# Performance work log

Measured on AMD Instinct MI355X. Metric: run time of the kernel, lower is better.

Reference implementation:

```python
import jax, jax.numpy as jnp
import numpy as np

B, T, E = 4, 2048, 1024
HS = 64            # attention_head_size
NH = E // HS       # num_heads = 16 (all heads share one weight set in the original)


def setup_inputs() -> dict:
    key = jax.random.key(0)
    ks = jax.random.split(key, 6)
    s = 0.02
    x = jax.random.normal(ks[0], (B, T, E), dtype=jnp.float32)
    Wq = jax.random.normal(ks[1], (E, HS), dtype=jnp.float32) * s
    Wk = jax.random.normal(ks[2], (E, HS), dtype=jnp.float32) * s
    Wv = jax.random.normal(ks[3], (E, HS), dtype=jnp.float32) * s
    Wp = jax.random.normal(ks[4], (E, E), dtype=jnp.float32) * s
    bp = jax.random.normal(ks[5], (E,), dtype=jnp.float32) * s
    return {"x": x, "Wq": Wq, "Wk": Wk, "Wv": Wv, "Wp": Wp, "bp": bp}


def reference(x, Wq, Wk, Wv, Wp, bp):
    # Single shared head (the torch module replicates one Head instance NH times).
    hs = Wq.shape[1]
    num_heads = Wp.shape[0] // hs
    q = jnp.einsum('bte,eh->bth', x, Wq)   # [B,T,HS]
    k = jnp.einsum('bte,eh->bth', x, Wk)
    v = jnp.einsum('bte,eh->bth', x, Wv)
    att = jnp.einsum('bqh,bkh->bqk', q, k) * (hs ** -0.5)  # [B,T,T]
    t = x.shape[1]
    causal = jnp.tril(jnp.ones((t, t), dtype=bool))
    att = jnp.where(causal, att, jnp.finfo(att.dtype).min)
    att = jax.nn.softmax(att, axis=-1)
    head = jnp.einsum('bqk,bkh->bqh', att, v)              # [B,T,HS]
    # Concat of identical head outputs == tile along feature dim.
    out = jnp.tile(head, (1, 1, num_heads))                # [B,T,E]
    out = jnp.einsum('bte,ef->btf', out, Wp) + bp          # output projection
    return out
```

## Files before the change

### kernel.cpp

```cpp
#include <hip/hip_runtime.h>
#include <hip/hip_bf16.h>

#define T_SEQ 2048
#define E_DIM 1024
#define HSZ   64
#define NBAT  4
#define QB    64
#define NQT   32

typedef __attribute__((ext_vector_type(8))) short short8;
typedef __attribute__((ext_vector_type(4))) float f32x4;

__device__ inline short f2bf(float f) {
  union { float f; unsigned u; } v; v.f = f;
  unsigned r = v.u + 0x7FFFu + ((v.u >> 16) & 1u);
  return (short)(r >> 16);
}

__global__ __launch_bounds__(256) void wpr_kernel(const float* __restrict__ Wp,
                                                  short* __restrict__ Wpb) {
  int idx = blockIdx.x * 256 + threadIdx.x;
  int f = idx & (E_DIM - 1);
  int j = idx >> 10;
  float s = 0.f;
#pragma unroll
  for (int h = 0; h < 16; ++h) s += Wp[(size_t)(h * HSZ + j) * E_DIM + f];
  Wpb[(size_t)f * HSZ + j] = f2bf(s);
}

__global__ __launch_bounds__(256) void wt_kernel(const float* __restrict__ Wq,
    const float* __restrict__ Wk, const float* __restrict__ Wv,
    short* __restrict__ Wt) {
  int idx = blockIdx.x * 256 + threadIdx.x;
  int kk = idx & 63;
  int tmp = idx >> 6;
  int kt = tmp / 192;
  int n = tmp - kt * 192;
  const float* W = (n < 64) ? Wq : (n < 128) ? Wk : Wv;
  Wt[idx] = f2bf(W[(size_t)(kt * 64 + kk) * HSZ + (n & 63)]);
}

__global__ __launch_bounds__(256) void qkv_mfma(const float* __restrict__ X,
    const short* __restrict__ Wt, short* __restrict__ Qo,
    short* __restrict__ Ko, short* __restrict__ Vt) {
  __shared__ short Xs[16 * 64];
  __shared__ short Ws[192 * 64];

  const int tid = threadIdx.x;
  const int m0 = blockIdx.x * 16;
  const int lane = tid & 63, w = tid >> 6;
  const int l15 = lane & 15, l4 = lane >> 4;

  f32x4 acc[3];
  acc[0] = (f32x4)0.f; acc[1] = (f32x4)0.f; acc[2] = (f32x4)0.f;

  for (int kt = 0; kt < 16; ++kt) {
    const int k0 = kt * 64;
    if (tid < 128) {
      int r = tid >> 3, c = tid & 7;
      const float* s = &X[(size_t)(m0 + r) * E_DIM + k0 + c * 8];
      float4 a = *(const float4*)s, d = *(const float4*)(s + 4);
      short8 f;
      f[0] = f2bf(a.x); f[1] = f2bf(a.y); f[2] = f2bf(a.z); f[3] = f2bf(a.w);
      f[4] = f2bf(d.x); f[5] = f2bf(d.y); f[6] = f2bf(d.z); f[7] = f2bf(d.w);
      *(short8*)&Xs[r * 64 + ((c ^ (r & 7)) * 8)] = f;
    }
    {
      const short* wsrc = Wt + (size_t)kt * 12288;
#pragma unroll
      for (int i = 0; i < 6; ++i) {
        int ci = tid + i * 256;
        int r = ci >> 3, c = ci & 7;
        short8 f = *(const short8*)&wsrc[ci * 8];
        *(short8*)&Ws[r * 64 + ((c ^ (r & 7)) * 8)] = f;
      }
    }
    __syncthreads();
#pragma unroll
    for (int ks = 0; ks < 2; ++ks) {
      short8 af = *(short8*)&Xs[l15 * 64 + (((ks * 4 + l4) ^ (l15 & 7)) * 8)];
#pragma unroll
      for (int i = 0; i < 3; ++i) {
        int n = (w * 3 + i) * 16 + l15;
        short8 bf = *(short8*)&Ws[n * 64 + (((ks * 4 + l4) ^ (n & 7)) * 8)];
        acc[i] = __builtin_amdgcn_mfma_f32_16x16x32_bf16(af, bf, acc[i], 0, 0, 0);
      }
    }
    __syncthreads();
  }

  const int b = m0 >> 11, t = m0 & 2047;
#pragma unroll
  for (int i = 0; i < 3; ++i) {
    const int nb = w * 3 + i;
    const int col = (nb & 3) * 16 + l15;
    const int sel = nb >> 2;
#pragma unroll
    for (int reg = 0; reg < 4; ++reg) {
      const int row = l4 * 4 + reg;
      short v = f2bf(acc[i][reg]);
      if (sel == 0)      Qo[(size_t)(m0 + row) * HSZ + col] = v;
      else if (sel == 1) Ko[(size_t)(m0 + row) * HSZ + col] = v;
      else               Vt[((size_t)b * HSZ + col) * T_SEQ + t + row] = v;
    }
  }
}

__global__ __launch_bounds__(256) void attn_part(const short* __restrict__ Q,
    const short* __restrict__ K, const short* __restrict__ Vt,
    float* __restrict__ Opart, float* __restrict__ mpart,
    float* __restrict__ lpart, int splits) {
  const int qt = blockIdx.x;
  const int sp = blockIdx.y;
  const int b  = blockIdx.z;
  const int ntile = qt + 1;
  const int t0 = (sp * ntile) / splits;
  const int t1 = ((sp + 1) * ntile) / splits;
  const int q0 = qt * QB;
  const int pidx = (b * NQT + qt) * splits + sp;
  float* Op = Opart + (size_t)pidx * QB * HSZ;
  float* mp = mpart + (size_t)pidx * QB;
  float* lp = lpart + (size_t)pidx * QB;
  const int tid = threadIdx.x;

  if (t0 >= t1) {
    if (tid < QB) { mp[tid] = -1e30f; lp[tid] = 0.f; }
    return;
  }

  const short* Qb  = Q  + (size_t)b * T_SEQ * HSZ;
  const short* Kb  = K  + (size_t)b * T_SEQ * HSZ;
  const short* Vtb = Vt + (size_t)b * HSZ * T_SEQ;

  __shared__ short Ks[64 * 64];
  __shared__ short Vs[64 * 64];
  __shared__ short Ps[4][16 * 64];

  const int lane = tid & 63;
  const int w    = tid >> 6;
  const int l15  = lane & 15;
  const int l4   = lane >> 4;

  short8 qf[2];
#pragma unroll
  for (int ks = 0; ks < 2; ++ks)
    qf[ks] = *(const short8*)&Qb[(size_t)(q0 + w * 16 + l15) * HSZ + ks * 32 + l4 * 8];

  f32x4 o[4];
  float m_[4], l_[4];
#pragma unroll
  for (int i = 0; i < 4; ++i) { o[i] = (f32x4)0.f; m_[i] = -1e30f; l_[i] = 0.f; }

  for (int kt = t0; kt < t1; ++kt) {
    const int kv0 = kt * 64;
#pragma unroll
    for (int ci = tid; ci < 512; ci += 256) {
      int r = ci >> 3, c = ci & 7;
      short8 f = *(const short8*)&Kb[(size_t)(kv0 + r) * HSZ + c * 8];
      *(short8*)&Ks[r * 64 + ((c ^ (r & 7)) * 8)] = f;
    }
#pragma unroll
    for (int ci = tid; ci < 512; ci += 256) {
      int r = ci >> 3, c = ci & 7;
      short8 f = *(const short8*)&Vtb[(size_t)r * T_SEQ + kv0 + c * 8];
      *(short8*)&Vs[r * 64 + ((c ^ (r & 7)) * 8)] = f;
    }
    __syncthreads();

    f32x4 sacc[4];
#pragma unroll
    for (int nb = 0; nb < 4; ++nb) sacc[nb] = (f32x4)0.f;
#pragma unroll
    for (int nb = 0; nb < 4; ++nb) {
      const int krow = nb * 16 + l15;
#pragma unroll
      for (int ks = 0; ks < 2; ++ks) {
        short8 kf = *(short8*)&Ks[krow * 64 + (((ks * 4 + l4) ^ (krow & 7)) * 8)];
        sacc[nb] = __builtin_amdgcn_mfma_f32_16x16x32_bf16(qf[ks], kf, sacc[nb],
                                                           0, 0, 0);
      }
    }

    const bool diag = (kt == qt);
#pragma unroll
    for (int reg = 0; reg < 4; ++reg) {
      const int grow = q0 + w * 16 + l4 * 4 + reg;
      float sv[4];
      float rmax = -1e30f;
#pragma unroll
      for (int nb = 0; nb < 4; ++nb) {
        sv[nb] = sacc[nb][reg] * 0.125f;
        if (diag && (kv0 + nb * 16 + l15 > grow)) sv[nb] = -1e30f;
        rmax = fmaxf(rmax, sv[nb]);
      }
#pragma unroll
      for (int d = 1; d < 16; d <<= 1) rmax = fmaxf(rmax, __shfl_xor(rmax, d));
      const float mn = fmaxf(m_[reg], rmax);
      const float sc = __expf(m_[reg] - mn);
      float rsum = 0.f;
#pragma unroll
      for (int nb = 0; nb < 4; ++nb) {
        sv[nb] = __expf(sv[nb] - mn);
        rsum += sv[nb];
      }
#pragma unroll
      for (int d = 1; d < 16; d <<= 1) rsum += __shfl_xor(rsum, d);
      l_[reg] = l_[reg] * sc + rsum;
      m_[reg] = mn;
#pragma unroll
      for (int hb = 0; hb < 4; ++hb) o[hb][reg] *= sc;
      const int prow = l4 * 4 + reg;
#pragma unroll
      for (int nb = 0; nb < 4; ++nb) {
        const int col = nb * 16 + l15;
        Ps[w][prow * 64 + (((col >> 3) ^ (prow & 7)) * 8) + (col & 7)] =
            f2bf(sv[nb]);
      }
    }

#pragma unroll
    for (int ks = 0; ks < 2; ++ks) {
      const int prow = l15;
      short8 pf = *(short8*)&Ps[w][prow * 64 + (((ks * 4 + l4) ^ (prow & 7)) * 8)];
#pragma unroll
      for (int hb = 0; hb < 4; ++hb) {
        const int vrow = hb * 16 + l15;
        short8 vf = *(short8*)&Vs[vrow * 64 + (((ks * 4 + l4) ^ (vrow & 7)) * 8)];
        o[hb] = __builtin_amdgcn_mfma_f32_16x16x32_bf16(pf, vf, o[hb], 0, 0, 0);
      }
    }
    __syncthreads();
  }

#pragma unroll
  for (int hb = 0; hb < 4; ++hb)
#pragma unroll
    for (int reg = 0; reg < 4; ++reg)
      Op[(size_t)(w * 16 + l4 * 4 + reg) * HSZ + hb * 16 + l15] = o[hb][reg];
  if (l15 == 0) {
#pragma unroll
    for (int reg = 0; reg < 4; ++reg) {
      mp[w * 16 + l4 * 4 + reg] = m_[reg];
      lp[w * 16 + l4 * 4 + reg] = l_[reg];
    }
  }
}

__global__ __launch_bounds__(256) void attn_combine(
    const float* __restrict__ Opart, const float* __restrict__ mpart,
    const float* __restrict__ lpart, short* __restrict__ Hd16, int splits) {
  const int qt = blockIdx.x, b = blockIdx.y;
  const int row = threadIdx.x >> 2;
  const int c0 = (threadIdx.x & 3) * 16;
  const int pbase = (b * NQT + qt) * splits;

  float M = -1e30f;
  for (int s = 0; s < splits; ++s)
    M = fmaxf(M, mpart[(size_t)(pbase + s) * QB + row]);

  float L = 0.f;
  float acc[16];
#pragma unroll
  for (int c = 0; c < 16; ++c) acc[c] = 0.f;

  for (int s = 0; s < splits; ++s) {
    const float ms = mpart[(size_t)(pbase + s) * QB + row];
    const float ls = lpart[(size_t)(pbase + s) * QB + row];
    const float w = __expf(ms - M);
    L += w * ls;
    const float* Op = Opart + ((size_t)(pbase + s) * QB + row) * HSZ + c0;
#pragma unroll
    for (int cc = 0; cc < 16; cc += 4) {
      float4 v = *(const float4*)&Op[cc];
      acc[cc + 0] += w * v.x; acc[cc + 1] += w * v.y;
      acc[cc + 2] += w * v.z; acc[cc + 3] += w * v.w;
    }
  }

  const float inv = 1.f / L;
  short* dst = Hd16 + ((size_t)b * T_SEQ + qt * QB + row) * HSZ + c0;
  short8 v0, v1;
#pragma unroll
  for (int cc = 0; cc < 8; ++cc) {
    v0[cc] = f2bf(acc[cc] * inv);
    v1[cc] = f2bf(acc[8 + cc] * inv);
  }
  *(short8*)dst = v0;
  *(short8*)(dst + 8) = v1;
}

__global__ __launch_bounds__(256) void proj_mfma(const short* __restrict__ Hd16,
    const short* __restrict__ Wpb, const float* __restrict__ bp,
    float* __restrict__ Out) {
  const int tid = threadIdx.x;
  const int lane = tid & 63, w = tid >> 6;
  const int l15 = lane & 15, l4 = lane >> 4;
  const int m0 = blockIdx.x * 64 + w * 16;
  const int n0 = blockIdx.y * 128;

  const short* asrc = &Hd16[(size_t)(m0 + l15) * HSZ + l4 * 8];
  short8 af0 = *(const short8*)asrc;
  short8 af1 = *(const short8*)(asrc + 32);

#pragma unroll
  for (int nb = 0; nb < 8; ++nb) {
    const int n = n0 + nb * 16 + l15;
    const short* bsrc = &Wpb[(size_t)n * HSZ + l4 * 8];
    short8 b0 = *(const short8*)bsrc;
    short8 b1 = *(const short8*)(bsrc + 32);
    f32x4 acc = (f32x4)0.f;
    acc = __builtin_amdgcn_mfma_f32_16x16x32_bf16(af0, b0, acc, 0, 0, 0);
    acc = __builtin_amdgcn_mfma_f32_16x16x32_bf16(af1, b1, acc, 0, 0, 0);
    const float bpv = bp[n];
#pragma unroll
    for (int reg = 0; reg < 4; ++reg)
      Out[(size_t)(m0 + l4 * 4 + reg) * E_DIM + n] = acc[reg] + bpv;
  }
}

extern "C" void kernel_launch(void* const* d_in, const int* in_sizes, int n_in,
                              void* d_out, int out_size, void* d_ws,
                              size_t ws_size, hipStream_t stream) {
  (void)in_sizes; (void)n_in; (void)out_size;
  const float* x  = (const float*)d_in[0];
  const float* Wq = (const float*)d_in[1];
  const float* Wk = (const float*)d_in[2];
  const float* Wv = (const float*)d_in[3];
  const float* Wp = (const float*)d_in[4];
  const float* bp = (const float*)d_in[5];
  float* out = (float*)d_out;

  float* ws   = (float*)d_ws;
  short* Qb16 = (short*)(ws);
  short* Kb16 = (short*)(ws + 262144);
  short* Vt16 = (short*)(ws + 524288);
  short* Hd16 = (short*)(ws + 786432);
  short* Wpb  = (short*)(ws + 1048576);
  short* Wt   = (short*)(ws + 1081344);
  const size_t base = 1179648;

  int splits = 8;
  const size_t per_split = (size_t)NBAT * NQT * (QB * HSZ + 2 * QB);
  while (splits > 1 && (base + per_split * splits) * 4 > ws_size) splits >>= 1;

  float* Opart = ws + base;
  float* mpart = Opart + (size_t)NBAT * NQT * splits * QB * HSZ;
  float* lpart = mpart + (size_t)NBAT * NQT * splits * QB;

  wpr_kernel<<<dim3(256), dim3(256), 0, stream>>>(Wp, Wpb);
  wt_kernel<<<dim3(768), dim3(256), 0, stream>>>(Wq, Wk, Wv, Wt);
  qkv_mfma<<<dim3(512), dim3(256), 0, stream>>>(x, Wt, Qb16, Kb16, Vt16);
  attn_part<<<dim3(NQT, splits, NBAT), dim3(256), 0, stream>>>(
      Qb16, Kb16, Vt16, Opart, mpart, lpart, splits);
  attn_combine<<<dim3(NQT, NBAT), dim3(256), 0, stream>>>(
      Opart, mpart, lpart, Hd16, splits);
  proj_mfma<<<dim3(128, 8), dim3(256), 0, stream>>>(Hd16, Wpb, bp, out);
}
```

Before: 150.3 us.

## Fuse pipeline into one cooperative persistent kernel with grid syncs

Merges the six separate kernels (weight prep, QKV projection, split attention, combine, output projection) into one cooperative kernel of 512 blocks. Grid-wide syncs separate the stages, and each block processes fixed work units per stage, with the attention units ordered so the longest query tiles start first. The aim is to remove per-launch overhead and idle gaps between launches. The cost is grid.sync overhead, load imbalance inside each stage, and occupancy limited to 2 blocks per CU. If the cooperative launch fails, a multi-kernel fallback runs, and it no longer shrinks the split count when the workspace is small.

```diff
diff --git a/kernel.cpp b/kernel.cpp
--- a/kernel.cpp
+++ b/kernel.cpp
@@ -1,5 +1,8 @@
 #include <hip/hip_runtime.h>
 #include <hip/hip_bf16.h>
+#include <hip/hip_cooperative_groups.h>
+
+namespace cg = cooperative_groups;
 
 #define T_SEQ 2048
 #define E_DIM 1024
@@ -7,6 +10,7 @@
 #define NBAT  4
 #define QB    64
 #define NQT   32
+#define SPL   8
 
 typedef __attribute__((ext_vector_type(8))) short short8;
 typedef __attribute__((ext_vector_type(4))) float f32x4;
@@ -17,37 +21,34 @@
   return (short)(r >> 16);
 }
 
-__global__ __launch_bounds__(256) void wpr_kernel(const float* __restrict__ Wp,
-                                                  short* __restrict__ Wpb) {
-  int idx = blockIdx.x * 256 + threadIdx.x;
-  int f = idx & (E_DIM - 1);
-  int j = idx >> 10;
-  float s = 0.f;
-#pragma unroll
-  for (int h = 0; h < 16; ++h) s += Wp[(size_t)(h * HSZ + j) * E_DIM + f];
-  Wpb[(size_t)f * HSZ + j] = f2bf(s);
-}
-
-__global__ __launch_bounds__(256) void wt_kernel(const float* __restrict__ Wq,
-    const float* __restrict__ Wk, const float* __restrict__ Wv,
+
+__device__ inline void prep_item(int idx, const float* __restrict__ Wp,
+    const float* __restrict__ Wq, const float* __restrict__ Wk,
+    const float* __restrict__ Wv, short* __restrict__ Wpb,
     short* __restrict__ Wt) {
-  int idx = blockIdx.x * 256 + threadIdx.x;
-  int kk = idx & 63;
-  int tmp = idx >> 6;
-  int kt = tmp / 192;
-  int n = tmp - kt * 192;
-  const float* W = (n < 64) ? Wq : (n < 128) ? Wk : Wv;
-  Wt[idx] = f2bf(W[(size_t)(kt * 64 + kk) * HSZ + (n & 63)]);
-}
-
-__global__ __launch_bounds__(256) void qkv_mfma(const float* __restrict__ X,
-    const short* __restrict__ Wt, short* __restrict__ Qo,
-    short* __restrict__ Ko, short* __restrict__ Vt) {
-  __shared__ short Xs[16 * 64];
-  __shared__ short Ws[192 * 64];
-
-  const int tid = threadIdx.x;
-  const int m0 = blockIdx.x * 16;
+  if (idx < 65536) {
+    int f = idx & (E_DIM - 1);
+    int j = idx >> 10;
+    float s = 0.f;
+#pragma unroll
+    for (int h = 0; h < 16; ++h) s += Wp[(size_t)(h * HSZ + j) * E_DIM + f];
+    Wpb[(size_t)f * HSZ + j] = f2bf(s);
+  } else {
+    int id2 = idx - 65536;
+    int kk = id2 & 63;
+    int tmp = id2 >> 6;
+    int kt = tmp / 192;
+    int n = tmp - kt * 192;
+    const float* W = (n < 64) ? Wq : (n < 128) ? Wk : Wv;
+    Wt[id2] = f2bf(W[(size_t)(kt * 64 + kk) * HSZ + (n & 63)]);
+  }
+}
+
+__device__ inline void qkv_tile(char* smem, int m0, int tid,
+    const float* __restrict__ X, const short* __restrict__ Wt,
+    short* __restrict__ Qo, short* __restrict__ Ko, short* __restrict__ Vt) {
+  short* Xs = (short*)smem;
+  short* Ws_ = (short*)(smem + 2048);
   const int lane = tid & 63, w = tid >> 6;
   const int l15 = lane & 15, l4 = lane >> 4;
 
@@ -72,7 +73,7 @@
         int ci = tid + i * 256;
         int r = ci >> 3, c = ci & 7;
         short8 f = *(const short8*)&wsrc[ci * 8];
-        *(short8*)&Ws[r * 64 + ((c ^ (r & 7)) * 8)] = f;
+        *(short8*)&Ws_[r * 64 + ((c ^ (r & 7)) * 8)] = f;
       }
     }
     __syncthreads();
@@ -82,7 +83,7 @@
 #pragma unroll
       for (int i = 0; i < 3; ++i) {
         int n = (w * 3 + i) * 16 + l15;
-        short8 bf = *(short8*)&Ws[n * 64 + (((ks * 4 + l4) ^ (n & 7)) * 8)];
+        short8 bf = *(short8*)&Ws_[n * 64 + (((ks * 4 + l4) ^ (n & 7)) * 8)];
         acc[i] = __builtin_amdgcn_mfma_f32_16x16x32_bf16(af, bf, acc[i], 0, 0, 0);
       }
     }
@@ -106,22 +107,22 @@
   }
 }
 
-__global__ __launch_bounds__(256) void attn_part(const short* __restrict__ Q,
-    const short* __restrict__ K, const short* __restrict__ Vt,
-    float* __restrict__ Opart, float* __restrict__ mpart,
-    float* __restrict__ lpart, int splits) {
-  const int qt = blockIdx.x;
-  const int sp = blockIdx.y;
-  const int b  = blockIdx.z;
+__device__ inline void attn_unit(char* smem, int u, int tid,
+    const short* __restrict__ Q, const short* __restrict__ K,
+    const short* __restrict__ Vt, float* __restrict__ Opart,
+    float* __restrict__ mpart, float* __restrict__ lpart) {
+  const int r_ = u & 255;
+  const int qt = NQT - 1 - (r_ & 31);
+  const int sp = (r_ >> 5) & 7;
+  const int b  = u >> 8;
   const int ntile = qt + 1;
-  const int t0 = (sp * ntile) / splits;
-  const int t1 = ((sp + 1) * ntile) / splits;
+  const int t0 = (sp * ntile) / SPL;
+  const int t1 = ((sp + 1) * ntile) / SPL;
   const int q0 = qt * QB;
-  const int pidx = (b * NQT + qt) * splits + sp;
+  const int pidx = (b * NQT + qt) * SPL + sp;
   float* Op = Opart + (size_t)pidx * QB * HSZ;
   float* mp = mpart + (size_t)pidx * QB;
   float* lp = lpart + (size_t)pidx * QB;
-  const int tid = threadIdx.x;
 
   if (t0 >= t1) {
     if (tid < QB) { mp[tid] = -1e30f; lp[tid] = 0.f; }
@@ -132,14 +133,12 @@
   const short* Kb  = K  + (size_t)b * T_SEQ * HSZ;
   const short* Vtb = Vt + (size_t)b * HSZ * T_SEQ;
 
-  __shared__ short Ks[64 * 64];
-  __shared__ short Vs[64 * 64];
-  __shared__ short Ps[4][16 * 64];
-
-  const int lane = tid & 63;
-  const int w    = tid >> 6;
-  const int l15  = lane & 15;
-  const int l4   = lane >> 4;
+  short* Ks = (short*)smem;
+  short* Vs = (short*)(smem + 8192);
+  short* Ps = (short*)(smem + 16384);
+
+  const int lane = tid & 63, w = tid >> 6;
+  const int l15 = lane & 15, l4 = lane >> 4;
 
   short8 qf[2];
 #pragma unroll
@@ -213,7 +212,7 @@
 #pragma unroll
       for (int nb = 0; nb < 4; ++nb) {
         const int col = nb * 16 + l15;
-        Ps[w][prow * 64 + (((col >> 3) ^ (prow & 7)) * 8) + (col & 7)] =
+        Ps[w * 1024 + prow * 64 + (((col >> 3) ^ (prow & 7)) * 8) + (col & 7)] =
             f2bf(sv[nb]);
       }
     }
@@ -221,7 +220,7 @@
 #pragma unroll
     for (int ks = 0; ks < 2; ++ks) {
       const int prow = l15;
-      short8 pf = *(short8*)&Ps[w][prow * 64 + (((ks * 4 + l4) ^ (prow & 7)) * 8)];
+      short8 pf = *(short8*)&Ps[w * 1024 + prow * 64 + (((ks * 4 + l4) ^ (prow & 7)) * 8)];
 #pragma unroll
       for (int hb = 0; hb < 4; ++hb) {
         const int vrow = hb * 16 + l15;
@@ -246,16 +245,17 @@
   }
 }
 
-__global__ __launch_bounds__(256) void attn_combine(
+__device__ inline void combine_unit(int cu, int tid,
     const float* __restrict__ Opart, const float* __restrict__ mpart,
-    const float* __restrict__ lpart, short* __restrict__ Hd16, int splits) {
-  const int qt = blockIdx.x, b = blockIdx.y;
-  const int row = threadIdx.x >> 2;
-  const int c0 = (threadIdx.x & 3) * 16;
-  const int pbase = (b * NQT + qt) * splits;
+    const float* __restrict__ lpart, short* __restrict__ Hd16) {
+  const int qt = cu & 31, b = cu >> 5;
+  const int row = tid >> 2;
+  const int c0 = (tid & 3) * 16;
+  const int pbase = (b * NQT + qt) * SPL;
 
   float M = -1e30f;
-  for (int s = 0; s < splits; ++s)
+#pragma unroll
+  for (int s = 0; s < SPL; ++s)
     M = fmaxf(M, mpart[(size_t)(pbase + s) * QB + row]);
 
   float L = 0.f;
@@ -263,17 +263,18 @@
 #pragma unroll
   for (int c = 0; c < 16; ++c) acc[c] = 0.f;
 
-  for (int s = 0; s < splits; ++s) {
+#pragma unroll
+  for (int s = 0; s < SPL; ++s) {
     const float ms = mpart[(size_t)(pbase + s) * QB + row];
     const float ls = lpart[(size_t)(pbase + s) * QB + row];
-    const float w = __expf(ms - M);
-    L += w * ls;
+    const float wg = __expf(ms - M);
+    L += wg * ls;
     const float* Op = Opart + ((size_t)(pbase + s) * QB + row) * HSZ + c0;
 #pragma unroll
     for (int cc = 0; cc < 16; cc += 4) {
       float4 v = *(const float4*)&Op[cc];
-      acc[cc + 0] += w * v.x; acc[cc + 1] += w * v.y;
-      acc[cc + 2] += w * v.z; acc[cc + 3] += w * v.w;
+      acc[cc + 0] += wg * v.x; acc[cc + 1] += wg * v.y;
+      acc[cc + 2] += wg * v.z; acc[cc + 3] += wg * v.w;
     }
   }
 
@@ -289,14 +290,13 @@
   *(short8*)(dst + 8) = v1;
 }
 
-__global__ __launch_bounds__(256) void proj_mfma(const short* __restrict__ Hd16,
-    const short* __restrict__ Wpb, const float* __restrict__ bp,
-    float* __restrict__ Out) {
-  const int tid = threadIdx.x;
+__device__ inline void proj_unit(int pu, int tid,
+    const short* __restrict__ Hd16, const short* __restrict__ Wpb,
+    const float* __restrict__ bp, float* __restrict__ Out) {
   const int lane = tid & 63, w = tid >> 6;
   const int l15 = lane & 15, l4 = lane >> 4;
-  const int m0 = blockIdx.x * 64 + w * 16;
-  const int n0 = blockIdx.y * 128;
+  const int m0 = (pu & 127) * 64 + w * 16;
+  const int n0 = (pu >> 7) * 128;
 
   const short* asrc = &Hd16[(size_t)(m0 + l15) * HSZ + l4 * 8];
   short8 af0 = *(const short8*)asrc;
@@ -318,10 +318,88 @@
   }
 }
 
+__global__ __launch_bounds__(256, 2) void mega_kernel(
+    const float* __restrict__ x, const float* __restrict__ Wq,
+    const float* __restrict__ Wk, const float* __restrict__ Wv,
+    const float* __restrict__ Wp, const float* __restrict__ bp,
+    float* __restrict__ out, float* __restrict__ ws) {
+  short* Qb16  = (short*)(ws);
+  short* Kb16  = (short*)(ws + 262144);
+  short* Vt16  = (short*)(ws + 524288);
+  short* Hd16  = (short*)(ws + 786432);
+  short* Wpb   = (short*)(ws + 1048576);
+  short* Wt    = (short*)(ws + 1081344);
+  float* Opart = ws + 1179648;
+  float* mpart = Opart + (size_t)NBAT * NQT * SPL * QB * HSZ;
+  float* lpart = mpart + (size_t)NBAT * NQT * SPL * QB;
+
+  cg::grid_group grid = cg::this_grid();
+  const int bid = blockIdx.x;
+  const int tid = threadIdx.x;
+
+  __shared__ __align__(16) char smem[26624];
+
+  prep_item(bid * 256 + tid, Wp, Wq, Wk, Wv, Wpb, Wt);
+  prep_item(131072 + bid * 256 + tid, Wp, Wq, Wk, Wv, Wpb, Wt);
+  __threadfence();
+  grid.sync();
+
+  qkv_tile(smem, bid * 16, tid, x, Wt, Qb16, Kb16, Vt16);
+  __threadfence();
+  grid.sync();
+
+  attn_unit(smem, bid, tid, Qb16, Kb16, Vt16, Opart, mpart, lpart);
+  __syncthreads();
+  attn_unit(smem, bid + 512, tid, Qb16, Kb16, Vt16, Opart, mpart, lpart);
+  __threadfence();
+  grid.sync();
+
+  if (bid < 128) combine_unit(bid, tid, Opart, mpart, lpart, Hd16);
+  __threadfence();
+  grid.sync();
+
+  proj_unit(bid, tid, Hd16, Wpb, bp, out);
+  proj_unit(bid + 512, tid, Hd16, Wpb, bp, out);
+}
+
+__global__ __launch_bounds__(256) void prep_kernel(const float* __restrict__ Wp,
+    const float* __restrict__ Wq, const float* __restrict__ Wk,
+    const float* __restrict__ Wv, short* __restrict__ Wpb,
+    short* __restrict__ Wt) {
+  prep_item(blockIdx.x * 256 + threadIdx.x, Wp, Wq, Wk, Wv, Wpb, Wt);
+}
+
+__global__ __launch_bounds__(256) void qkv_kernel(const float* __restrict__ X,
+    const short* __restrict__ Wt, short* __restrict__ Qo,
+    short* __restrict__ Ko, short* __restrict__ Vt) {
+  __shared__ __align__(16) char smem[26624];
+  qkv_tile(smem, blockIdx.x * 16, threadIdx.x, X, Wt, Qo, Ko, Vt);
+}
+
+__global__ __launch_bounds__(256) void attn_kernel(const short* __restrict__ Q,
+    const short* __restrict__ K, const short* __restrict__ Vt,
+    float* __restrict__ Opart, float* __restrict__ mpart,
+    float* __restrict__ lpart) {
+  __shared__ __align__(16) char smem[24576];
+  attn_unit(smem, blockIdx.x, threadIdx.x, Q, K, Vt, Opart, mpart, lpart);
+}
+
+__global__ __launch_bounds__(256) void combine_kernel(
+    const float* __restrict__ Opart, const float* __restrict__ mpart,
+    const float* __restrict__ lpart, short* __restrict__ Hd16) {
+  combine_unit(blockIdx.x, threadIdx.x, Opart, mpart, lpart, Hd16);
+}
+
+__global__ __launch_bounds__(256) void proj_kernel(const short* __restrict__ Hd16,
+    const short* __restrict__ Wpb, const float* __restrict__ bp,
+    float* __restrict__ Out) {
+  proj_unit(blockIdx.x, threadIdx.x, Hd16, Wpb, bp, Out);
+}
+
 extern "C" void kernel_launch(void* const* d_in, const int* in_sizes, int n_in,
                               void* d_out, int out_size, void* d_ws,
                               size_t ws_size, hipStream_t stream) {
-  (void)in_sizes; (void)n_in; (void)out_size;
+  (void)in_sizes; (void)n_in; (void)out_size; (void)ws_size;
   const float* x  = (const float*)d_in[0];
   const float* Wq = (const float*)d_in[1];
   const float* Wk = (const float*)d_in[2];
@@ -329,30 +407,32 @@
   const float* Wp = (const float*)d_in[4];
   const float* bp = (const float*)d_in[5];
   float* out = (float*)d_out;
-
-  float* ws   = (float*)d_ws;
-  short* Qb16 = (short*)(ws);
-  short* Kb16 = (short*)(ws + 262144);
-  short* Vt16 = (short*)(ws + 524288);
-  short* Hd16 = (short*)(ws + 786432);
-  short* Wpb  = (short*)(ws + 1048576);
-  short* Wt   = (short*)(ws + 1081344);
-  const size_t base = 1179648;
-
-  int splits = 8;
-  const size_t per_split = (size_t)NBAT * NQT * (QB * HSZ + 2 * QB);
-  while (splits > 1 && (base + per_split * splits) * 4 > ws_size) splits >>= 1;
-
-  float* Opart = ws + base;
-  float* mpart = Opart + (size_t)NBAT * NQT * splits * QB * HSZ;
-  float* lpart = mpart + (size_t)NBAT * NQT * splits * QB;
-
-  wpr_kernel<<<dim3(256), dim3(256), 0, stream>>>(Wp, Wpb);
-  wt_kernel<<<dim3(768), dim3(256), 0, stream>>>(Wq, Wk, Wv, Wt);
-  qkv_mfma<<<dim3(512), dim3(256), 0, stream>>>(x, Wt, Qb16, Kb16, Vt16);
-  attn_part<<<dim3(NQT, splits, NBAT), dim3(256), 0, stream>>>(
-      Qb16, Kb16, Vt16, Opart, mpart, lpart, splits);
-  attn_combine<<<dim3(NQT, NBAT), dim3(256), 0, stream>>>(
-      Opart, mpart, lpart, Hd16, splits);
-  proj_mfma<<<dim3(128, 8), dim3(256), 0, stream>>>(Hd16, Wpb, bp, out);
-}
+  float* wsf = (float*)d_ws;
+
+  const float* xa = x; const float* wqa = Wq; const float* wka = Wk;
+  const float* wva = Wv; const float* wpa = Wp; const float* bpa = bp;
+  float* outa = out; float* wsa = wsf;
+  void* args[] = {(void*)&xa, (void*)&wqa, (void*)&wka, (void*)&wva,
+                  (void*)&wpa, (void*)&bpa, (void*)&outa, (void*)&wsa};
+  hipError_t e = hipLaunchCooperativeKernel((void*)mega_kernel, dim3(512),
+                                            dim3(256), args, 0, stream);
+  if (e != hipSuccess) {
+    short* Qb16  = (short*)(wsf);
+    short* Kb16  = (short*)(wsf + 262144);
+    short* Vt16  = (short*)(wsf + 524288);
+    short* Hd16  = (short*)(wsf + 786432);
+    short* Wpb   = (short*)(wsf + 1048576);
+    short* Wt    = (short*)(wsf + 1081344);
+    float* Opart = wsf + 1179648;
+    float* mpart = Opart + (size_t)NBAT * NQT * SPL * QB * HSZ;
+    float* lpart = mpart + (size_t)NBAT * NQT * SPL * QB;
+
+    prep_kernel<<<dim3(1024), dim3(256), 0, stream>>>(Wp, Wq, Wk, Wv, Wpb, Wt);
+    qkv_kernel<<<dim3(512), dim3(256), 0, stream>>>(x, Wt, Qb16, Kb16, Vt16);
+    attn_kernel<<<dim3(1024), dim3(256), 0, stream>>>(Qb16, Kb16, Vt16,
+                                                      Opart, mpart, lpart);
+    combine_kernel<<<dim3(128), dim3(256), 0, stream>>>(Opart, mpart, lpart,
+                                                        Hd16);
+    proj_kernel<<<dim3(1024), dim3(256), 0, stream>>>(Hd16, Wpb, bp, out);
+  }
+}
```

Result: slower. 585.7 us (+289.8%).
